# Performance work log

Measured on AMD Instinct MI355X. Metric: run time of the kernel, lower is better.

The kernel has to match this reference:

```python
import jax, jax.numpy as jnp
import numpy as np

C = 512; H = 64; W = 64; STRIDE = 16; NA = 9; IMG = 1024
PRE_NMS = 6000; POST_NMS = 300; NMS_T = 0.7; MIN_SIZE = 16.0
BBOX_CLIP = float(np.log(1000.0 / 16.0))  # standard dw/dh clamp for exp() safety


def _make_anchors():
    # 3 scales x 3 aspect ratios on a stride-16 grid -> (H*W*9, 4) xyxy anchors
    scales = np.array([128.0, 256.0, 512.0])
    ratios = np.array([0.5, 1.0, 2.0])
    hs = (scales[:, None] * np.sqrt(ratios)[None, :]).ravel()
    ws = (scales[:, None] / np.sqrt(ratios)[None, :]).ravel()
    yy, xx = np.meshgrid((np.arange(H) + 0.5) * STRIDE, (np.arange(W) + 0.5) * STRIDE, indexing='ij')
    ctr = np.stack([xx.ravel(), yy.ravel()], -1)            # (HW, 2) centers
    wh = np.stack([ws, hs], -1)                              # (9, 2)
    anc = np.concatenate([ctr[:, None, :] - 0.5 * wh[None], ctr[:, None, :] + 0.5 * wh[None]], -1)
    return anc.reshape(-1, 4).astype(np.float32)             # (HW*9, 4)


def setup_inputs() -> dict:
    key = jax.random.key(0)
    k = jax.random.split(key, 4)
    return {
        'feature_map': jax.random.normal(k[0], (1, C, H, W), jnp.float32),
        'anchors': jnp.asarray(_make_anchors()),
        'image_shape': jnp.array([IMG, IMG], jnp.int32),
        'conv1_w': 0.01 * jax.random.normal(k[1], (C, C, 3, 3), jnp.float32),
        'conv1_b': jnp.zeros((C,), jnp.float32),
        'cls_w': 0.01 * jax.random.normal(k[2], (NA, C, 1, 1), jnp.float32),
        'cls_b': jnp.zeros((NA,), jnp.float32),
        'box_w': 0.01 * jax.random.normal(k[3], (NA * 4, C, 1, 1), jnp.float32),
        'box_b': jnp.zeros((NA * 4,), jnp.float32),
    }


def _conv(x, w, b):
    dn = ('NCHW', 'OIHW', 'NCHW')
    return jax.lax.conv_general_dilated(x, w, (1, 1), 'SAME', dimension_numbers=dn) + b[None, :, None, None]


def _decode_boxes(deltas, anchors):
    aw = anchors[:, 2] - anchors[:, 0]
    ah = anchors[:, 3] - anchors[:, 1]
    ax = anchors[:, 0] + 0.5 * aw
    ay = anchors[:, 1] + 0.5 * ah
    dx, dy, dw, dh = deltas[:, 0], deltas[:, 1], deltas[:, 2], deltas[:, 3]
    dw = jnp.minimum(dw, BBOX_CLIP)
    dh = jnp.minimum(dh, BBOX_CLIP)
    px = dx * aw + ax
    py = dy * ah + ay
    pw = jnp.exp(dw) * aw
    ph = jnp.exp(dh) * ah
    return jnp.stack([px - 0.5 * pw, py - 0.5 * ph, px + 0.5 * pw, py + 0.5 * ph], -1)


def _pairwise_iou(a, b):
    area_a = (a[:, 2] - a[:, 0]) * (a[:, 3] - a[:, 1])
    area_b = (b[:, 2] - b[:, 0]) * (b[:, 3] - b[:, 1])
    lt = jnp.maximum(a[:, None, :2], b[None, :, :2])
    rb = jnp.minimum(a[:, None, 2:], b[None, :, 2:])
    wh = jnp.clip(rb - lt, 0.0)
    inter = wh[..., 0] * wh[..., 1]
    union = area_a[:, None] + area_b[None, :] - inter
    return jnp.where(union > 0, inter / union, 0.0)


def reference(feature_map, anchors, image_shape, conv1_w, conv1_b, cls_w, cls_b, box_w, box_b):
    # conv head
    y = jax.nn.relu(_conv(feature_map, conv1_w, conv1_b))
    scores = _conv(y, cls_w, cls_b).reshape(-1)            # (H*W*9,)  torch .view(-1) order
    deltas = _conv(y, box_w, box_b).reshape(-1, 4)         # (H*W*9, 4) torch .reshape(-1,4) order
    preds = _decode_boxes(deltas, anchors)

    # filter_proposals: sigmoid -> topk 6000 -> clamp -> min-size -> NMS(0.7) -> top 300
    s = jax.nn.sigmoid(scores)
    topv, topi = jax.lax.top_k(s, PRE_NMS)                  # sorted descending
    b = preds[topi]
    h_img = image_shape[0].astype(jnp.float32)
    w_img = image_shape[1].astype(jnp.float32)
    b = jnp.stack([jnp.clip(b[:, 0], 0.0, w_img), jnp.clip(b[:, 1], 0.0, h_img),
                   jnp.clip(b[:, 2], 0.0, w_img), jnp.clip(b[:, 3], 0.0, h_img)], -1)
    valid = ((b[:, 2] - b[:, 0]) >= MIN_SIZE) & ((b[:, 3] - b[:, 1]) >= MIN_SIZE)

    iou = _pairwise_iou(b, b)                               # (6000, 6000)
    idx = jnp.arange(PRE_NMS)

    def body(i, keep):  # greedy NMS in score order (boxes already sorted desc)
        sup = (iou[i] > NMS_T) & keep[i] & (idx > i)
        return keep & (~sup)

    keep = jax.lax.fori_loop(0, PRE_NMS, body, valid)
    fs = jnp.where(keep, topv, -1.0)                        # suppressed/invalid -> sentinel
    sc, i2 = jax.lax.top_k(fs, POST_NMS)
    return b[i2], sc
```

## Files before the change

kernel.cpp:

```cpp
#include <hip/hip_runtime.h>
#include <hip/hip_bf16.h>

typedef unsigned int u32;
typedef unsigned long long u64;
typedef float v2f __attribute__((ext_vector_type(2)));
typedef float v4f __attribute__((ext_vector_type(4)));

#define OFF_Y      0ull
#define OFF_WT     8388608ull
#define OFF_ZPART  8388608ull
#define OFF_SCORES 11337728ull
#define OFF_DRAW   11485184ull
#define OFF_HIST   12075008ull
#define OFF_TOPV   12665344ull
#define OFF_BOXES  12714496ull
#define OFF_VW     12812800ull
#define OFF_MASK   12813824ull

#define NS     36864
#define PRE    6000
#define POST   300
#define SORTN  8192
#define MROW   96

__global__ __launch_bounds__(256) void k_wtrans(const float* __restrict__ gw,
                                                float* __restrict__ wT) {
    int o = blockIdx.x * 256 + threadIdx.x;
    if (o >= 512 * 512 * 9) return;
    int ci = o / 4608;
    int r = o - ci * 4608;
    int k = r >> 9;
    int co = r & 511;
    wT[o] = gw[co * 4608 + ci * 9 + k];
}

#define CI 16
#define XROW 66
#define CHUNK_ELEMS (CI * 3 * XROW)
#define STAGE_IT 13
__global__ __launch_bounds__(256, 4) void k_conv1(const float* __restrict__ x,
                                                  const float* __restrict__ wT,
                                                  const float* __restrict__ gb,
                                                  float* __restrict__ y) {
    __shared__ float xs[CHUNK_ELEMS];
    const int t = threadIdx.x;
    const int tx = t & 63;
    const int wv = __builtin_amdgcn_readfirstlane(t >> 6);
    const int cob = (blockIdx.x & 15) << 5;
    const int h0 = blockIdx.x >> 4;
    const int co_base = cob + (wv << 3);

    int offs[STAGE_IT];
    u32 vmask = 0;
#pragma unroll
    for (int u = 0; u < STAGE_IT; ++u) {
        int idx = t + u * 256;
        offs[u] = 0;
        if (idx < CHUNK_ELEMS) {
            int ci = idx / (3 * XROW);
            int rem = idx - ci * (3 * XROW);
            int row = rem / XROW;
            int col = rem - row * XROW;
            int gr = h0 + row - 1, gc = col - 1;
            if ((unsigned)gr < 64u && (unsigned)gc < 64u) {
                offs[u] = ci * 4096 + (gr << 6) + gc;
                vmask |= 1u << u;
            }
        }
    }

    v2f acc2[4];
#pragma unroll
    for (int j = 0; j < 4; ++j) acc2[j] = (v2f){0.f, 0.f};

    float st[STAGE_IT];
#pragma unroll
    for (int u = 0; u < STAGE_IT; ++u)
        st[u] = (vmask >> u & 1) ? x[offs[u]] : 0.f;

#pragma unroll 1
    for (int cc = 0; cc < 32; ++cc) {
        if (cc) __syncthreads();
#pragma unroll
        for (int u = 0; u < STAGE_IT; ++u) {
            int idx = t + u * 256;
            if (idx < CHUNK_ELEMS) xs[idx] = st[u];
        }
        __syncthreads();
        if (cc + 1 < 32) {
            const float* xsrc = x + (cc + 1) * CI * 4096;
#pragma unroll
            for (int u = 0; u < STAGE_IT; ++u)
                st[u] = (vmask >> u & 1) ? xsrc[offs[u]] : 0.f;
        }

        const int cig0 = cc * CI;
#pragma unroll 2
        for (int ci = 0; ci < CI; ++ci) {
            float xr[9];
            {
                const float* xp = xs + ci * (3 * XROW) + tx;
#pragma unroll
                for (int r = 0; r < 3; ++r) {
                    xr[r * 3 + 0] = xp[r * XROW + 0];
                    xr[r * 3 + 1] = xp[r * XROW + 1];
                    xr[r * 3 + 2] = xp[r * XROW + 2];
                }
            }
            const float* wk = wT + (size_t)(cig0 + ci) * 4608 + co_base;
#pragma unroll
            for (int k = 0; k < 9; ++k) {
                v4f wa = *(const v4f*)(wk + k * 512);
                v4f wb = *(const v4f*)(wk + k * 512 + 4);
                float xv = xr[k];
                v2f xp2 = {xv, xv};
                acc2[0] = __builtin_elementwise_fma(__builtin_shufflevector(wa, wa, 0, 1), xp2, acc2[0]);
                acc2[1] = __builtin_elementwise_fma(__builtin_shufflevector(wa, wa, 2, 3), xp2, acc2[1]);
                acc2[2] = __builtin_elementwise_fma(__builtin_shufflevector(wb, wb, 0, 1), xp2, acc2[2]);
                acc2[3] = __builtin_elementwise_fma(__builtin_shufflevector(wb, wb, 2, 3), xp2, acc2[3]);
            }
        }
    }

#pragma unroll
    for (int j = 0; j < 4; ++j) {
        int co0 = co_base + 2 * j;
        float v0 = acc2[j].x + gb[co0];
        float v1 = acc2[j].y + gb[co0 + 1];
        v0 = v0 > 0.f ? v0 : 0.f;
        v1 = v1 > 0.f ? v1 : 0.f;
        y[co0 * 4096 + (h0 << 6) + tx] = v0;
        y[(co0 + 1) * 4096 + (h0 << 6) + tx] = v1;
    }
}

__global__ __launch_bounds__(256) void k_heads_part(const float* __restrict__ y,
                                                    const float* __restrict__ cw,
                                                    const float* __restrict__ bw,
                                                    float* __restrict__ zpart,
                                                    u32* __restrict__ hist) {
    __shared__ __align__(16) float ys[64][132];
    const int t = threadIdx.x;
    {
        int hb = blockIdx.x << 9;
        hist[hb + t] = 0u;
        hist[hb + 256 + t] = 0u;
    }
    const int px = t & 63;
    const int gu = __builtin_amdgcn_readfirstlane(t >> 6);
    const int px0 = (blockIdx.x & 63) << 6;
    const int q = blockIdx.x >> 6;
    const int cib = q << 7;
    const int nch = (gu == 0) ? 12 : 11;

    const float* wrow[12];
#pragma unroll
    for (int j = 0; j < 12; ++j) {
        int ch = gu + 4 * j;
        if (ch < 9) wrow[j] = cw + ch * 512;
        else if (ch < 45) wrow[j] = bw + (ch - 9) * 512;
        else wrow[j] = cw;
    }
    float acc[12];
#pragma unroll
    for (int j = 0; j < 12; ++j) acc[j] = 0.f;

    for (int idx = t; idx < 128 * 64; idx += 256) {
        int ci = idx >> 6;
        int pp = idx & 63;
        ys[pp][ci] = y[(cib + ci) * 4096 + px0 + pp];
    }
    __syncthreads();

#pragma unroll 1
    for (int cq = 0; cq < 32; ++cq) {
        float4 yv = *(const float4*)&ys[px][cq << 2];
        float4 wv[12];
#pragma unroll
        for (int j = 0; j < 12; ++j)
            if (j < nch) wv[j] = *(const float4*)(wrow[j] + cib + (cq << 2));
#pragma unroll
        for (int j = 0; j < 12; ++j)
            if (j < nch)
                acc[j] += wv[j].x * yv.x + wv[j].y * yv.y + wv[j].z * yv.z + wv[j].w * yv.w;
    }
    for (int j = 0; j < nch; ++j) {
        int ch = gu + 4 * j;
        zpart[((q * 45 + ch) << 12) + px0 + px] = acc[j];
    }
}

__global__ __launch_bounds__(256) void k_hreduce(const float* __restrict__ zpart,
                                                 const float* __restrict__ cb,
                                                 const float* __restrict__ bb,
                                                 float* __restrict__ scores,
                                                 float* __restrict__ draw,
                                                 u32* __restrict__ hist) {
    int i = blockIdx.x * 256 + threadIdx.x;
    if (i >= 45 * 4096) return;
    int ch = i >> 12;
    int sp = i & 4095;
    float z = zpart[((0 * 45 + ch) << 12) + sp] + zpart[((1 * 45 + ch) << 12) + sp] +
              zpart[((2 * 45 + ch) << 12) + sp] + zpart[((3 * 45 + ch) << 12) + sp];
    if (ch < 9) {
        z += cb[ch];
        float s = 1.f / (1.f + expf(-z));
        scores[(ch << 12) + sp] = s;
        u32 sb = __float_as_uint(s);
        atomicAdd(&hist[sb >> 13], 1u);
    } else {
        z += bb[ch - 9];
        draw[((ch - 9) << 12) + sp] = z;
    }
}

__global__ __launch_bounds__(1024) void k_select(const u32* __restrict__ hist,
                                                 const float* __restrict__ scores,
                                                 const float* __restrict__ draw,
                                                 const float* __restrict__ anchors,
                                                 const int* __restrict__ ishape,
                                                 float* __restrict__ boxes,
                                                 float* __restrict__ topv,
                                                 u64* __restrict__ vw) {
    __shared__ u32 csum[1024];
    __shared__ u32 suf[1024];
    __shared__ u64 sk[SORTN];
    __shared__ int sel_s, cnt_s;
    const int t = threadIdx.x;

    u32 s = 0;
    const u32* hp = hist + t * 128;
    for (int i = 0; i < 128; ++i) s += hp[i];
    csum[t] = s;
    suf[t] = s;
    if (t == 0) cnt_s = 0;
    __syncthreads();
    for (int off = 1; off < 1024; off <<= 1) {
        u32 v = suf[t] + ((t + off < 1024) ? suf[t + off] : 0u);
        __syncthreads();
        suf[t] = v;
        __syncthreads();
    }
    u32 above = suf[t] - csum[t];
    if (above < (u32)PRE && suf[t] >= (u32)PRE) {
        u32 run = above;
        int bstar = t * 128;
        u32 found = 0;
        for (int b2 = 127; b2 >= 0; --b2) {
            u32 c = hp[b2];
            if (!found && run + c >= (u32)PRE) { bstar = t * 128 + b2; found = 1; }
            if (!found) run += c;
        }
        sel_s = bstar;
    }
    for (int i = t; i < SORTN; i += 1024) sk[i] = 0;
    __syncthreads();

    const int sel = sel_s;
    for (int i = t; i < NS; i += 1024) {
        u32 sb = __float_as_uint(scores[i]);
        if ((int)(sb >> 13) >= sel) {
            int p = atomicAdd(&cnt_s, 1);
            if (p < SORTN) sk[p] = ((u64)sb << 32) | (u32)(~i);
        }
    }
    __syncthreads();

    const int base = t << 3;
    u64 a[8];
    {
#pragma unroll
        for (int u = 0; u < 8; ++u) a[u] = sk[base + u];
#pragma unroll
        for (int k = 2; k <= 8; k <<= 1) {
#pragma unroll
            for (int j = k >> 1; j > 0; j >>= 1) {
#pragma unroll
                for (int u = 0; u < 8; ++u) {
                    if ((u & j) == 0) {
                        int l = u | j;
                        bool up = (((base + u) & k) == 0);
                        u64 x0 = a[u], x1 = a[l];
                        if (up ? (x0 < x1) : (x0 > x1)) { a[u] = x1; a[l] = x0; }
                    }
                }
            }
        }
#pragma unroll
        for (int u = 0; u < 8; ++u) sk[base + u] = a[u];
        __syncthreads();
    }
    for (int k = 16; k <= SORTN; k <<= 1) {
        for (int j = k >> 1; j >= 8; j >>= 1) {
#pragma unroll
            for (int s2 = 0; s2 < 4; ++s2) {
                int pidx = t + (s2 << 10);
                int i = ((pidx & ~(j - 1)) << 1) | (pidx & (j - 1));
                int l = i | j;
                u64 x0 = sk[i], x1 = sk[l];
                bool up = ((i & k) == 0);
                if (up ? (x0 < x1) : (x0 > x1)) { sk[i] = x1; sk[l] = x0; }
            }
            __syncthreads();
        }
#pragma unroll
        for (int u = 0; u < 8; ++u) a[u] = sk[base + u];
        {
            bool up = ((base & k) == 0);
#pragma unroll
            for (int j = 4; j > 0; j >>= 1) {
#pragma unroll
                for (int u = 0; u < 8; ++u) {
                    if ((u & j) == 0) {
                        int l = u | j;
                        u64 x0 = a[u], x1 = a[l];
                        if (up ? (x0 < x1) : (x0 > x1)) { a[u] = x1; a[l] = x0; }
                    }
                }
            }
        }
#pragma unroll
        for (int u = 0; u < 8; ++u) sk[base + u] = a[u];
        __syncthreads();
    }

    const float wimg = (float)ishape[1], himg = (float)ishape[0];
#pragma unroll 1
    for (int s2 = 0; s2 < 6; ++s2) {
        int r = (s2 << 10) + t;
        bool valid = false;
        if (r < PRE) {
            u64 key = sk[r];
            u32 sb = (u32)(key >> 32);
            int i = (int)(~(u32)key);
            topv[r] = __uint_as_float(sb);
            int c = i >> 10;
            int t4 = i & 1023;
            float4 d4 = *(const float4*)(draw + c * 4096 + (t4 << 2));
            float4 a4 = *(const float4*)(anchors + i * 4);
            float aw = a4.z - a4.x, ah = a4.w - a4.y;
            float ax = a4.x + 0.5f * aw, ay = a4.y + 0.5f * ah;
            const float CLIPV = (float)4.135166556742356;
            float dw = fminf(d4.z, CLIPV);
            float dh = fminf(d4.w, CLIPV);
            float px = d4.x * aw + ax, py = d4.y * ah + ay;
            float pw = expf(dw) * aw, ph = expf(dh) * ah;
            float x1 = fminf(fmaxf(px - 0.5f * pw, 0.f), wimg);
            float y1 = fminf(fmaxf(py - 0.5f * ph, 0.f), himg);
            float x2 = fminf(fmaxf(px + 0.5f * pw, 0.f), wimg);
            float y2 = fminf(fmaxf(py + 0.5f * ph, 0.f), himg);
            valid = (x2 - x1 >= 16.f) && (y2 - y1 >= 16.f);
            *(float4*)(boxes + r * 4) = make_float4(x1, y1, x2, y2);
        }
        u64 bm = __ballot(valid);
        if ((t & 63) == 0) vw[(s2 << 4) + (t >> 6)] = bm;
    }
}

__global__ __launch_bounds__(256) void k_mask(const float* __restrict__ boxes,
                                              u64* __restrict__ mask) {
    __shared__ float4 cbx[16 * 65];
    const int t = threadIdx.x;
    const int r0 = blockIdx.x << 4;
    const int row = r0 + (t >> 4);
    const int wloc = t & 15;
    float4 rb = *(const float4*)(boxes + row * 4);
    float area_a = (rb.z - rb.x) * (rb.w - rb.y);
    for (int chunk = 0; chunk < 6; ++chunk) {
        int j0c = chunk << 10;
        for (int idx = t; idx < 1024; idx += 256) {
            int j = j0c + idx;
            float4 v = make_float4(0.f, 0.f, 0.f, 0.f);
            if (j < PRE) v = *(const float4*)(boxes + j * 4);
            cbx[(idx >> 6) * 65 + (idx & 63)] = v;
        }
        __syncthreads();
        u64 bits = 0;
        const float4* cbr = cbx + wloc * 65;
        for (int b = 0; b < 64; ++b) {
            int j = j0c + (wloc << 6) + b;
            float4 ob = cbr[b];
            float area_b = (ob.z - ob.x) * (ob.w - ob.y);
            float ltx = fmaxf(rb.x, ob.x), lty = fmaxf(rb.y, ob.y);
            float rbx = fminf(rb.z, ob.z), rby = fminf(rb.w, ob.w);
            float wx = fmaxf(rbx - ltx, 0.f), wy = fmaxf(rby - lty, 0.f);
            float inter = wx * wy;
            float uni = area_a + area_b - inter;
            float iou = (uni > 0.f) ? (inter / uni) : 0.f;
            if (iou > 0.7f && j > row && j < PRE) bits |= (1ull << b);
        }
        mask[(size_t)row * MROW + (chunk << 4) + wloc] = bits;
        __syncthreads();
    }
}

__global__ __launch_bounds__(320) void k_nms_out(const u64* __restrict__ mask,
                                                 const u64* __restrict__ vw,
                                                 const float* __restrict__ boxes,
                                                 const float* __restrict__ topv,
                                                 float* __restrict__ out) {
    __shared__ u64 rem[MROW];
    __shared__ u64 rows16[16][MROW];
    __shared__ u64 kws[MROW];
    __shared__ int keepl[POST];
    const int tid = threadIdx.x;
    for (int i = tid; i < MROW; i += 320) { rem[i] = 0ull; kws[i] = 0ull; }
    __syncthreads();
    int kc = 0;
    bool done = false;
    for (int w = 0; w < 94 && !done; ++w) {
        u64 aw = vw[w] & ~rem[w];
        u64 kwbits = 0;
        while (aw != 0ull && !done) {
            int bq[16];
            u64 tmp = aw;
#pragma unroll
            for (int q2 = 0; q2 < 16; ++q2) {
                bq[q2] = tmp ? __builtin_ctzll(tmp) : 64;
                tmp &= tmp - 1;
            }
#pragma unroll
            for (int u = 0; u < 5; ++u) {
                int i = tid + u * 320;
                if (i < 16 * MROW) {
                    int q2 = i / MROW;
                    int ww = i - q2 * MROW;
                    if (bq[q2] < 64)
                        rows16[q2][ww] = mask[(size_t)((w << 6) + bq[q2]) * MROW + ww];
                }
            }
            __syncthreads();
            for (int q2 = 0; q2 < 16; ++q2) {
                int b = bq[q2];
                if (b >= 64) break;
                if (!((aw >> b) & 1ull)) continue;
                if (tid == 0) keepl[kc] = (w << 6) + b;
                kc++;
                kwbits |= (1ull << b);
                if (kc >= POST) { done = true; break; }
                if (tid < MROW) rem[tid] |= rows16[q2][tid];
                aw &= ~rows16[q2][w];
                aw &= ~(1ull << b);
            }
            __syncthreads();
        }
        if (tid == 0) kws[w] = kwbits;
        __syncthreads();
    }
    __syncthreads();

    int j = tid;
    if (j >= POST) return;
    int kc2 = kc;
    int r;
    float sc;
    if (j < kc2) {
        r = keepl[j];
        sc = topv[r];
    } else {
        int target = j - kc2;
        r = PRE - 1;
        int cum = 0;
        for (int w = 0; w < 94; ++w) {
            u64 kb = kws[w];
            int nvalid = (w < 93) ? 64 : 48;
            u64 vmask2 = (nvalid == 64) ? ~0ull : ((1ull << nvalid) - 1ull);
            u64 nk = (~kb) & vmask2;
            int c = __popcll(nk);
            if (cum + c > target) {
                int need = target - cum;
                u64 m = nk;
                for (int q = 0; q < need; ++q) m &= (m - 1);
                r = (w << 6) + __builtin_ctzll(m);
                break;
            }
            cum += c;
        }
        sc = -1.0f;
    }
    out[j * 4 + 0] = boxes[r * 4 + 0];
    out[j * 4 + 1] = boxes[r * 4 + 1];
    out[j * 4 + 2] = boxes[r * 4 + 2];
    out[j * 4 + 3] = boxes[r * 4 + 3];
    out[1200 + j] = sc;
}

extern "C" void kernel_launch(void* const* d_in, const int* in_sizes, int n_in,
                              void* d_out, int out_size, void* d_ws, size_t ws_size,
                              hipStream_t stream) {
    const float* x = (const float*)d_in[0];
    const float* anchors = (const float*)d_in[1];
    const int* ishape = (const int*)d_in[2];
    const float* c1w = (const float*)d_in[3];
    const float* c1b = (const float*)d_in[4];
    const float* clw = (const float*)d_in[5];
    const float* clb = (const float*)d_in[6];
    const float* bxw = (const float*)d_in[7];
    const float* bxb = (const float*)d_in[8];

    char* ws = (char*)d_ws;
    float* y      = (float*)(ws + OFF_Y);
    float* wT     = (float*)(ws + OFF_WT);
    float* zpart  = (float*)(ws + OFF_ZPART);
    float* scores = (float*)(ws + OFF_SCORES);
    float* draw   = (float*)(ws + OFF_DRAW);
    u32*   hist   = (u32*)(ws + OFF_HIST);
    float* topv   = (float*)(ws + OFF_TOPV);
    float* boxes  = (float*)(ws + OFF_BOXES);
    u64*   vw     = (u64*)(ws + OFF_VW);
    u64*   mask   = (u64*)(ws + OFF_MASK);

    k_wtrans<<<(512 * 512 * 9 + 255) / 256, 256, 0, stream>>>(c1w, wT);
    k_conv1<<<1024, 256, 0, stream>>>(x, wT, c1b, y);
    k_heads_part<<<256, 256, 0, stream>>>(y, clw, bxw, zpart, hist);
    k_hreduce<<<(45 * 4096 + 255) / 256, 256, 0, stream>>>(zpart, clb, bxb, scores, draw, hist);
    k_select<<<1, 1024, 0, stream>>>(hist, scores, draw, anchors, ishape, boxes, topv, vw);
    k_mask<<<PRE / 16, 256, 0, stream>>>(boxes, mask);
    k_nms_out<<<1, 320, 0, stream>>>(mask, vw, boxes, topv, (float*)d_out);
}
```

Baseline: 712.6 us.

## Compute two output rows per conv thread and repack weights contiguously per group

```diff
diff --git a/kernel.cpp b/kernel.cpp
--- a/kernel.cpp
+++ b/kernel.cpp
@@ -27,18 +27,22 @@
                                                 float* __restrict__ wT) {
     int o = blockIdx.x * 256 + threadIdx.x;
     if (o >= 512 * 512 * 9) return;
-    int ci = o / 4608;
-    int r = o - ci * 4608;
-    int k = r >> 9;
-    int co = r & 511;
+    int cor = o & 7;
+    int t9 = o >> 3;
+    int k = t9 % 9;
+    int t64 = t9 / 9;
+    int cog = t64 & 63;
+    int ci = t64 >> 6;
+    int co = (cog << 3) | cor;
     wT[o] = gw[co * 4608 + ci * 9 + k];
 }
 
 #define CI 16
 #define XROW 66
-#define CHUNK_ELEMS (CI * 3 * XROW)
-#define STAGE_IT 13
-__global__ __launch_bounds__(256, 4) void k_conv1(const float* __restrict__ x,
+#define XR0WS 4
+#define CHUNK_ELEMS (CI * XR0WS * XROW)
+#define STAGE_IT 17
+__global__ __launch_bounds__(256, 2) void k_conv1(const float* __restrict__ x,
                                                   const float* __restrict__ wT,
                                                   const float* __restrict__ gb,
                                                   float* __restrict__ y) {
@@ -49,6 +53,7 @@
     const int cob = (blockIdx.x & 15) << 5;
     const int h0 = blockIdx.x >> 4;
     const int co_base = cob + (wv << 3);
+    const int wgrp = (cob >> 3) + wv;
 
     int offs[STAGE_IT];
     u32 vmask = 0;
@@ -57,11 +62,11 @@
         int idx = t + u * 256;
         offs[u] = 0;
         if (idx < CHUNK_ELEMS) {
-            int ci = idx / (3 * XROW);
-            int rem = idx - ci * (3 * XROW);
+            int ci = idx / (XR0WS * XROW);
+            int rem = idx - ci * (XR0WS * XROW);
             int row = rem / XROW;
             int col = rem - row * XROW;
-            int gr = h0 + row - 1, gc = col - 1;
+            int gr = (h0 << 1) + row - 1, gc = col - 1;
             if ((unsigned)gr < 64u && (unsigned)gc < 64u) {
                 offs[u] = ci * 4096 + (gr << 6) + gc;
                 vmask |= 1u << u;
@@ -69,9 +74,11 @@
         }
     }
 
-    v2f acc2[4];
-#pragma unroll
-    for (int j = 0; j < 4; ++j) acc2[j] = (v2f){0.f, 0.f};
+    v2f acc2[2][4];
+#pragma unroll
+    for (int r = 0; r < 2; ++r)
+#pragma unroll
+        for (int j = 0; j < 4; ++j) acc2[r][j] = (v2f){0.f, 0.f};
 
     float st[STAGE_IT];
 #pragma unroll
@@ -97,40 +104,50 @@
         const int cig0 = cc * CI;
 #pragma unroll 2
         for (int ci = 0; ci < CI; ++ci) {
-            float xr[9];
+            float xr[XR0WS][3];
             {
-                const float* xp = xs + ci * (3 * XROW) + tx;
-#pragma unroll
-                for (int r = 0; r < 3; ++r) {
-                    xr[r * 3 + 0] = xp[r * XROW + 0];
-                    xr[r * 3 + 1] = xp[r * XROW + 1];
-                    xr[r * 3 + 2] = xp[r * XROW + 2];
+                const float* xp = xs + ci * (XR0WS * XROW) + tx;
+#pragma unroll
+                for (int r = 0; r < XR0WS; ++r) {
+                    xr[r][0] = xp[r * XROW + 0];
+                    xr[r][1] = xp[r * XROW + 1];
+                    xr[r][2] = xp[r * XROW + 2];
                 }
             }
-            const float* wk = wT + (size_t)(cig0 + ci) * 4608 + co_base;
+            const v4f* w4 = (const v4f*)(wT + (size_t)(((cig0 + ci) << 6) + wgrp) * 72);
 #pragma unroll
             for (int k = 0; k < 9; ++k) {
-                v4f wa = *(const v4f*)(wk + k * 512);
-                v4f wb = *(const v4f*)(wk + k * 512 + 4);
-                float xv = xr[k];
-                v2f xp2 = {xv, xv};
-                acc2[0] = __builtin_elementwise_fma(__builtin_shufflevector(wa, wa, 0, 1), xp2, acc2[0]);
-                acc2[1] = __builtin_elementwise_fma(__builtin_shufflevector(wa, wa, 2, 3), xp2, acc2[1]);
-                acc2[2] = __builtin_elementwise_fma(__builtin_shufflevector(wb, wb, 0, 1), xp2, acc2[2]);
-                acc2[3] = __builtin_elementwise_fma(__builtin_shufflevector(wb, wb, 2, 3), xp2, acc2[3]);
-            }
-        }
-    }
-
-#pragma unroll
-    for (int j = 0; j < 4; ++j) {
-        int co0 = co_base + 2 * j;
-        float v0 = acc2[j].x + gb[co0];
-        float v1 = acc2[j].y + gb[co0 + 1];
-        v0 = v0 > 0.f ? v0 : 0.f;
-        v1 = v1 > 0.f ? v1 : 0.f;
-        y[co0 * 4096 + (h0 << 6) + tx] = v0;
-        y[(co0 + 1) * 4096 + (h0 << 6) + tx] = v1;
+                v4f wa = w4[2 * k];
+                v4f wb = w4[2 * k + 1];
+                const int kr = k / 3, kc = k % 3;
+                float x0 = xr[kr][kc];
+                float x1 = xr[kr + 1][kc];
+                v2f p0 = {x0, x0};
+                v2f p1 = {x1, x1};
+                acc2[0][0] = __builtin_elementwise_fma(__builtin_shufflevector(wa, wa, 0, 1), p0, acc2[0][0]);
+                acc2[0][1] = __builtin_elementwise_fma(__builtin_shufflevector(wa, wa, 2, 3), p0, acc2[0][1]);
+                acc2[0][2] = __builtin_elementwise_fma(__builtin_shufflevector(wb, wb, 0, 1), p0, acc2[0][2]);
+                acc2[0][3] = __builtin_elementwise_fma(__builtin_shufflevector(wb, wb, 2, 3), p0, acc2[0][3]);
+                acc2[1][0] = __builtin_elementwise_fma(__builtin_shufflevector(wa, wa, 0, 1), p1, acc2[1][0]);
+                acc2[1][1] = __builtin_elementwise_fma(__builtin_shufflevector(wa, wa, 2, 3), p1, acc2[1][1]);
+                acc2[1][2] = __builtin_elementwise_fma(__builtin_shufflevector(wb, wb, 0, 1), p1, acc2[1][2]);
+                acc2[1][3] = __builtin_elementwise_fma(__builtin_shufflevector(wb, wb, 2, 3), p1, acc2[1][3]);
+            }
+        }
+    }
+
+#pragma unroll
+    for (int r = 0; r < 2; ++r) {
+#pragma unroll
+        for (int j = 0; j < 4; ++j) {
+            int co0 = co_base + 2 * j;
+            float v0 = acc2[r][j].x + gb[co0];
+            float v1 = acc2[r][j].y + gb[co0 + 1];
+            v0 = v0 > 0.f ? v0 : 0.f;
+            v1 = v1 > 0.f ? v1 : 0.f;
+            y[co0 * 4096 + (h0 << 7) + (r << 6) + tx] = v0;
+            y[(co0 + 1) * 4096 + (h0 << 7) + (r << 6) + tx] = v1;
+        }
     }
 }
 
@@ -511,7 +528,7 @@
     u64*   mask   = (u64*)(ws + OFF_MASK);
 
     k_wtrans<<<(512 * 512 * 9 + 255) / 256, 256, 0, stream>>>(c1w, wT);
-    k_conv1<<<1024, 256, 0, stream>>>(x, wT, c1b, y);
+    k_conv1<<<512, 256, 0, stream>>>(x, wT, c1b, y);
     k_heads_part<<<256, 256, 0, stream>>>(y, clw, bxw, zpart, hist);
     k_hreduce<<<(45 * 4096 + 255) / 256, 256, 0, stream>>>(zpart, clb, bxb, scores, draw, hist);
     k_select<<<1, 1024, 0, stream>>>(hist, scores, draw, anchors, ishape, boxes, topv, vw);
```

Measured after the change: 952.8 us. 33.7% more time.

## Stage conv weights through LDS with block-contiguous transposed layout

Applied to the files above, without the earlier changes.

```diff
diff --git a/kernel.cpp b/kernel.cpp
--- a/kernel.cpp
+++ b/kernel.cpp
@@ -27,10 +27,13 @@
                                                 float* __restrict__ wT) {
     int o = blockIdx.x * 256 + threadIdx.x;
     if (o >= 512 * 512 * 9) return;
-    int ci = o / 4608;
-    int r = o - ci * 4608;
-    int k = r >> 9;
-    int co = r & 511;
+    int c = o & 31;
+    int t1 = o >> 5;
+    int k = t1 % 9;
+    int t2 = t1 / 9;
+    int cb = t2 & 15;
+    int ci = t2 >> 4;
+    int co = (cb << 5) | c;
     wT[o] = gw[co * 4608 + ci * 9 + k];
 }
 
@@ -38,15 +41,19 @@
 #define XROW 66
 #define CHUNK_ELEMS (CI * 3 * XROW)
 #define STAGE_IT 13
+#define WCHUNK (CI * 288)
+#define WSTAGE_IT 18
 __global__ __launch_bounds__(256, 4) void k_conv1(const float* __restrict__ x,
                                                   const float* __restrict__ wT,
                                                   const float* __restrict__ gb,
                                                   float* __restrict__ y) {
     __shared__ float xs[CHUNK_ELEMS];
+    __shared__ float wlds[WCHUNK];
     const int t = threadIdx.x;
     const int tx = t & 63;
     const int wv = __builtin_amdgcn_readfirstlane(t >> 6);
-    const int cob = (blockIdx.x & 15) << 5;
+    const int cb = blockIdx.x & 15;
+    const int cob = cb << 5;
     const int h0 = blockIdx.x >> 4;
     const int co_base = cob + (wv << 3);
 
@@ -68,15 +75,25 @@
             }
         }
     }
+    int wgoff[WSTAGE_IT];
+#pragma unroll
+    for (int u = 0; u < WSTAGE_IT; ++u) {
+        int idx = t + u * 256;
+        wgoff[u] = idx + (idx / 288) * 4320 + cb * 288;
+    }
 
     v2f acc2[4];
 #pragma unroll
     for (int j = 0; j < 4; ++j) acc2[j] = (v2f){0.f, 0.f};
 
     float st[STAGE_IT];
+    float stw[WSTAGE_IT];
 #pragma unroll
     for (int u = 0; u < STAGE_IT; ++u)
         st[u] = (vmask >> u & 1) ? x[offs[u]] : 0.f;
+#pragma unroll
+    for (int u = 0; u < WSTAGE_IT; ++u)
+        stw[u] = wT[wgoff[u]];
 
 #pragma unroll 1
     for (int cc = 0; cc < 32; ++cc) {
@@ -86,15 +103,21 @@
             int idx = t + u * 256;
             if (idx < CHUNK_ELEMS) xs[idx] = st[u];
         }
+#pragma unroll
+        for (int u = 0; u < WSTAGE_IT; ++u)
+            wlds[t + u * 256] = stw[u];
         __syncthreads();
         if (cc + 1 < 32) {
             const float* xsrc = x + (cc + 1) * CI * 4096;
 #pragma unroll
             for (int u = 0; u < STAGE_IT; ++u)
                 st[u] = (vmask >> u & 1) ? xsrc[offs[u]] : 0.f;
-        }
-
-        const int cig0 = cc * CI;
+            const float* wsrc = wT + (size_t)(cc + 1) * (CI * 4608);
+#pragma unroll
+            for (int u = 0; u < WSTAGE_IT; ++u)
+                stw[u] = wsrc[wgoff[u]];
+        }
+
 #pragma unroll 2
         for (int ci = 0; ci < CI; ++ci) {
             float xr[9];
@@ -107,11 +130,11 @@
                     xr[r * 3 + 2] = xp[r * XROW + 2];
                 }
             }
-            const float* wk = wT + (size_t)(cig0 + ci) * 4608 + co_base;
+            const float* wk = wlds + ci * 288 + (wv << 3);
 #pragma unroll
             for (int k = 0; k < 9; ++k) {
-                v4f wa = *(const v4f*)(wk + k * 512);
-                v4f wb = *(const v4f*)(wk + k * 512 + 4);
+                v4f wa = *(const v4f*)(wk + k * 32);
+                v4f wb = *(const v4f*)(wk + k * 32 + 4);
                 float xv = xr[k];
                 v2f xp2 = {xv, xv};
                 acc2[0] = __builtin_elementwise_fma(__builtin_shufflevector(wa, wa, 0, 1), xp2, acc2[0]);
```

After: 801.4 us. 12.5% more time.
